# Kernel tuning notes

Measured on AMD Instinct MI355X. Metric: run time of the kernel, lower is better.

## Reference

```python
import jax, jax.numpy as jnp
import numpy as np

B, T, V, E, H = 4096, 80, 80, 8, 256  # batch, seq_len, num_classes/vocab, embed dim, n_hidden
FORGET_BIAS = 1.0  # tf BasicLSTMCell default


def lstm_layer(x, W, b):
    """Run one BasicLSTMCell layer over time. x: [B, T, D]; W: [D+H, 4H]; b: [4H].
    TF BasicLSTMCell gate order is (i, j, f, o); new_c = c*sig(f+fb) + sig(i)*tanh(j)."""
    Bsz = x.shape[0]

    def step(carry, xt):
        c, h = carry
        gates = jnp.concatenate([xt, h], axis=-1) @ W + b  # [B, 4H]
        i, j, f, o = jnp.split(gates, 4, axis=-1)
        c = c * jax.nn.sigmoid(f + FORGET_BIAS) + jax.nn.sigmoid(i) * jnp.tanh(j)
        h = jnp.tanh(c) * jax.nn.sigmoid(o)
        return (c, h), h

    init = (jnp.zeros((Bsz, H), x.dtype), jnp.zeros((Bsz, H), x.dtype))
    _, hs = jax.lax.scan(step, init, jnp.swapaxes(x, 0, 1))  # hs: [T, B, H]
    return jnp.swapaxes(hs, 0, 1)  # [B, T, H]


def setup_inputs() -> dict:
    key = jax.random.key(0)
    ks = jax.random.split(key, 8)
    features = jax.random.randint(ks[0], (B, T), 0, V, dtype=jnp.int32)
    labels = jax.random.randint(ks[1], (B,), 0, V, dtype=jnp.int32)
    emb = jax.random.normal(ks[2], (V, E), dtype=jnp.float32) * 0.1  # trainable=False in original
    W1 = jax.random.normal(ks[3], (E + H, 4 * H), dtype=jnp.float32) * 0.05
    b1 = jnp.zeros((4 * H,), jnp.float32)
    W2 = jax.random.normal(ks[4], (H + H, 4 * H), dtype=jnp.float32) * 0.05
    b2 = jnp.zeros((4 * H,), jnp.float32)
    Wd = jax.random.normal(ks[5], (H, V), dtype=jnp.float32) * 0.05
    bd = jnp.zeros((V,), jnp.float32)
    return {"features": features, "labels": labels, "emb": emb,
            "W1": W1, "b1": b1, "W2": W2, "b2": b2, "Wd": Wd, "bd": bd}


def reference(features, labels, emb, W1, b1, W2, b2, Wd, bd):
    x = emb[features]                     # [B, T, E] embedding lookup
    h1 = lstm_layer(x, W1, b1)            # [B, T, H]
    h2 = lstm_layer(h1, W2, b2)           # [B, T, H]
    pred = h2[:, -1, :] @ Wd + bd         # [B, V] logits from last timestep
    y = jax.nn.one_hot(labels, V, dtype=pred.dtype)
    loss = jnp.mean(jnp.sum(-y * jax.nn.log_softmax(pred, axis=-1), axis=-1))
    return loss
```

## Files before the change

### kernel.cpp

```cpp
#include <hip/hip_runtime.h>
#include <math.h>

#define B_SZ 4096
#define T_SZ 80
#define V_SZ 80
#define E_SZ 8
#define H_SZ 256
#define G4   1024

typedef __attribute__((ext_vector_type(8))) short short8;
typedef __attribute__((ext_vector_type(4))) float f32x4;

__device__ __forceinline__ float sigm(float x) {
    return 1.f / (1.f + __expf(-x));
}
__device__ __forceinline__ float tanhfast(float x) {
    x = fminf(fmaxf(x, -15.f), 15.f);
    float t = __expf(-2.f * x);
    return (1.f - t) / (1.f + t);
}
__device__ __forceinline__ ushort f2bf(float f) {
    unsigned u = __float_as_uint(f);
    u = (u + 0x7fffu + ((u >> 16) & 1u)) >> 16;
    return (ushort)u;
}

__global__ __launch_bounds__(256) void g1_kernel(const float* __restrict__ emb,
                                                 const float* __restrict__ W1,
                                                 const float* __restrict__ b1,
                                                 float* __restrict__ G1) {
    int idx = blockIdx.x * 256 + threadIdx.x;
    if (idx >= V_SZ * G4) return;
    int v = idx >> 10, col = idx & 1023;
    float g = b1[col];
#pragma unroll
    for (int e = 0; e < E_SZ; e++)
        g += emb[v * E_SZ + e] * W1[e * G4 + col];
    G1[idx] = g;
}

__global__ __launch_bounds__(256) void wtrans(const float* __restrict__ src, int k0,
                                              int Kshift, ushort* __restrict__ out) {
    const int K = 1 << Kshift;
    int idx = blockIdx.x * 256 + threadIdx.x;
    int n = idx >> Kshift, k = idx & (K - 1);
    out[idx] = f2bf(src[(size_t)(k0 + k) * G4 + n]);
}

__global__ __launch_bounds__(256) void wdtrans(const float* __restrict__ src,
                                               ushort* __restrict__ out) {
    int idx = blockIdx.x * 256 + threadIdx.x;
    if (idx >= V_SZ * H_SZ) return;
    int v = idx >> 8, h = idx & 255;
    out[idx] = f2bf(src[h * V_SZ + v]);
}

__global__ __launch_bounds__(256) void lstm_fused(
    const ushort* __restrict__ A1h, int Kend1,
    const int*   __restrict__ feat,
    const float* __restrict__ G1,
    float* __restrict__ c1, ushort* __restrict__ h1out,
    const ushort* __restrict__ A2x, const ushort* __restrict__ A2h, int Kend2,
    const float* __restrict__ b2,
    float* __restrict__ c2, ushort* __restrict__ h2out,
    const ushort* __restrict__ W1t, const ushort* __restrict__ W2t) {

    const int z = blockIdx.z;
    const int Kend = z ? Kend2 : Kend1;
    if (Kend < 0) return;
    const int K = z ? 512 : 256;
    const ushort* __restrict__ Wt = z ? W2t : W1t;

    __shared__ ushort As[2][128 * 40];
    __shared__ ushort Ws[2][128 * 40];

    const int tid = threadIdx.x;
    const int w = tid >> 6, l = tid & 63;
    const int l15 = l & 15, l4 = l >> 4;
    const int m0 = blockIdx.x * 128;
    const int h0 = blockIdx.y * 32;

    const int row0 = tid >> 2, c40 = tid & 3;
    const int row1 = row0 + 64;
    const int ncol0 = (row0 >> 5) * 256 + h0 + (row0 & 31);
    const int ncol1 = (row1 >> 5) * 256 + h0 + (row1 & 31);
    const size_t wbase0 = (size_t)ncol0 * K + c40 * 8;
    const size_t wbase1 = (size_t)ncol1 * K + c40 * 8;
    const int lA0 = row0 * 40 + c40 * 8, lA1 = row1 * 40 + c40 * 8;

    const int aoff0 = (w * 32 + l15) * 40 + l4 * 8;
    const int aoff1 = aoff0 + 16 * 40;
    const int boff  = l15 * 40 + l4 * 8;

    f32x4 acc[2][8];
    const f32x4 zero4 = {0.f, 0.f, 0.f, 0.f};
#pragma unroll
    for (int fg = 0; fg < 2; fg++)
#pragma unroll
        for (int cf = 0; cf < 8; cf++) acc[fg][cf] = zero4;

    auto loadTile = [&](int kt, short8& a0, short8& a1, short8& w0, short8& w1) {
        const ushort* Asrc; int kl;
        if (!z)            { Asrc = A1h; kl = kt; }
        else if (kt < 256) { Asrc = A2x; kl = kt; }
        else               { Asrc = A2h; kl = kt - 256; }
        a0 = *(const short8*)(Asrc + (size_t)(m0 + row0) * H_SZ + kl + c40 * 8);
        a1 = *(const short8*)(Asrc + (size_t)(m0 + row1) * H_SZ + kl + c40 * 8);
        w0 = *(const short8*)(Wt + wbase0 + kt);
        w1 = *(const short8*)(Wt + wbase1 + kt);
    };

    short8 ga0, ga1, gw0, gw1;
    if (Kend > 0) {
        loadTile(0, ga0, ga1, gw0, gw1);
        *(short8*)(As[0] + lA0) = ga0;
        *(short8*)(As[0] + lA1) = ga1;
        *(short8*)(Ws[0] + lA0) = gw0;
        *(short8*)(Ws[0] + lA1) = gw1;
        if (Kend > 32) loadTile(32, ga0, ga1, gw0, gw1);
        __syncthreads();
    }

    int cur = 0;
    for (int kt = 0; kt < Kend; kt += 32) {
        short8 a0 = *(const short8*)(As[cur] + aoff0);
        short8 a1 = *(const short8*)(As[cur] + aoff1);
        short8 bq[8];
#pragma unroll
        for (int cf = 0; cf < 8; cf++)
            bq[cf] = *(const short8*)(Ws[cur] + boff + cf * 640);

        __builtin_amdgcn_s_setprio(1);
#pragma unroll
        for (int cf = 0; cf < 8; cf++) {
            acc[0][cf] = __builtin_amdgcn_mfma_f32_16x16x32_bf16(a0, bq[cf], acc[0][cf], 0, 0, 0);
            acc[1][cf] = __builtin_amdgcn_mfma_f32_16x16x32_bf16(a1, bq[cf], acc[1][cf], 0, 0, 0);
        }
        __builtin_amdgcn_s_setprio(0);

        if (kt + 32 < Kend) {
            *(short8*)(As[cur ^ 1] + lA0) = ga0;
            *(short8*)(As[cur ^ 1] + lA1) = ga1;
            *(short8*)(Ws[cur ^ 1] + lA0) = gw0;
            *(short8*)(Ws[cur ^ 1] + lA1) = gw1;
            if (kt + 64 < Kend) loadTile(kt + 64, ga0, ga1, gw0, gw1);
        }
        __syncthreads();
        cur ^= 1;
    }

    float* __restrict__ cbuf = z ? c2 : c1;
    ushort* __restrict__ hout = z ? h2out : h1out;
    const bool cz = z ? (Kend == 256) : (Kend == 0);

#pragma unroll
    for (int fg = 0; fg < 2; fg++) {
#pragma unroll
        for (int r = 0; r < 4; r++) {
            const int grow = m0 + w * 32 + fg * 16 + l4 * 4 + r;
            const float* gb = z ? b2 : (G1 + (size_t)feat[(size_t)grow * T_SZ] * G4);
#pragma unroll
            for (int h16 = 0; h16 < 2; h16++) {
                const int hcol = h0 + h16 * 16 + l15;
                float gi = acc[fg][0 + h16][r] + gb[hcol];
                float gj = acc[fg][2 + h16][r] + gb[256 + hcol];
                float gf = acc[fg][4 + h16][r] + gb[512 + hcol];
                float go = acc[fg][6 + h16][r] + gb[768 + hcol];
                const size_t ci = (size_t)grow * H_SZ + hcol;
                float cp = cz ? 0.f : cbuf[ci];
                float cn = cp * sigm(gf + 1.f) + sigm(gi) * tanhfast(gj);
                float hn = tanhfast(cn) * sigm(go);
                cbuf[ci] = cn;
                hout[ci] = f2bf(hn);
            }
        }
    }
}

__global__ __launch_bounds__(256) void dense_loss(const ushort* __restrict__ h2,
                                                  const ushort* __restrict__ WdT,
                                                  const float* __restrict__ bd,
                                                  const int* __restrict__ labels,
                                                  float* __restrict__ out) {
    const int tid = threadIdx.x;
    const int w = tid >> 6, l = tid & 63;
    const int l15 = l & 15, l4 = l >> 4;
    const int m0 = blockIdx.x * 64 + w * 16;

    f32x4 acc[5];
    const f32x4 zero4 = {0.f, 0.f, 0.f, 0.f};
#pragma unroll
    for (int cf = 0; cf < 5; cf++) acc[cf] = zero4;

    for (int kt = 0; kt < 256; kt += 32) {
        short8 a = *(const short8*)(h2 + (size_t)(m0 + l15) * H_SZ + l4 * 8 + kt);
#pragma unroll
        for (int cf = 0; cf < 5; cf++) {
            short8 b = *(const short8*)(WdT + (size_t)(cf * 16 + l15) * H_SZ + l4 * 8 + kt);
            acc[cf] = __builtin_amdgcn_mfma_f32_16x16x32_bf16(a, b, acc[cf], 0, 0, 0);
        }
    }
#pragma unroll
    for (int cf = 0; cf < 5; cf++) {
        float bv = bd[cf * 16 + l15];
#pragma unroll
        for (int r = 0; r < 4; r++) acc[cf][r] += bv;
    }

#pragma unroll
    for (int r = 0; r < 4; r++) {
        const int row = m0 + l4 * 4 + r;
        float mx = acc[0][r];
#pragma unroll
        for (int cf = 1; cf < 5; cf++) mx = fmaxf(mx, acc[cf][r]);
#pragma unroll
        for (int msk = 1; msk < 16; msk <<= 1)
            mx = fmaxf(mx, __shfl_xor(mx, msk, 64));
        float s = 0.f;
#pragma unroll
        for (int cf = 0; cf < 5; cf++) s += __expf(acc[cf][r] - mx);
#pragma unroll
        for (int msk = 1; msk < 16; msk <<= 1)
            s += __shfl_xor(s, msk, 64);
        const int lab = labels[row];
        float pl = 0.f;
#pragma unroll
        for (int cf = 0; cf < 5; cf++)
            pl += (cf * 16 + l15 == lab) ? acc[cf][r] : 0.f;
#pragma unroll
        for (int msk = 1; msk < 16; msk <<= 1)
            pl += __shfl_xor(pl, msk, 64);
        if (l15 == 0)
            atomicAdd(out, (logf(s) + mx - pl) * (1.0f / B_SZ));
    }
}

extern "C" void kernel_launch(void* const* d_in, const int* in_sizes, int n_in,
                              void* d_out, int out_size, void* d_ws, size_t ws_size,
                              hipStream_t stream) {
    const int*   features = (const int*)d_in[0];
    const int*   labels   = (const int*)d_in[1];
    const float* emb      = (const float*)d_in[2];
    const float* W1       = (const float*)d_in[3];
    const float* b1       = (const float*)d_in[4];
    const float* W2       = (const float*)d_in[5];
    const float* b2       = (const float*)d_in[6];
    const float* Wd       = (const float*)d_in[7];
    const float* bd       = (const float*)d_in[8];
    float* out = (float*)d_out;

    char* base = (char*)d_ws;
    float*  G1v = (float*)base;                      base += (size_t)V_SZ * G4 * 4;
    float*  c1  = (float*)base;                      base += (size_t)B_SZ * H_SZ * 4;
    float*  c2  = (float*)base;                      base += (size_t)B_SZ * H_SZ * 4;
    ushort* h1b[2]; ushort* h2b[2];
    h1b[0] = (ushort*)base;                          base += (size_t)B_SZ * H_SZ * 2;
    h1b[1] = (ushort*)base;                          base += (size_t)B_SZ * H_SZ * 2;
    h2b[0] = (ushort*)base;                          base += (size_t)B_SZ * H_SZ * 2;
    h2b[1] = (ushort*)base;                          base += (size_t)B_SZ * H_SZ * 2;
    ushort* W1t = (ushort*)base;                     base += (size_t)G4 * H_SZ * 2;
    ushort* W2t = (ushort*)base;                     base += (size_t)G4 * 2 * H_SZ * 2;
    ushort* WdT = (ushort*)base;                     base += (size_t)V_SZ * H_SZ * 2;

    (void)hipMemsetAsync(d_out, 0, sizeof(float), stream);
    g1_kernel<<<(V_SZ * G4 + 255) / 256, 256, 0, stream>>>(emb, W1, b1, G1v);
    wtrans<<<(G4 * 256) / 256, 256, 0, stream>>>(W1, E_SZ, 8, W1t);
    wtrans<<<(G4 * 512) / 256, 256, 0, stream>>>(W2, 0, 9, W2t);
    wdtrans<<<(V_SZ * H_SZ + 255) / 256, 256, 0, stream>>>(Wd, WdT);

    dim3 grid(B_SZ / 128, H_SZ / 32, 2), blk(256);
    for (int t = 0; t <= T_SZ; t++) {
        const int Kend1 = (t < T_SZ) ? (t ? 256 : 0) : -1;
        const int Kend2 = (t >= 1) ? ((t >= 2) ? 512 : 256) : -1;
        lstm_fused<<<grid, blk, 0, stream>>>(
            (t && t < T_SZ) ? h1b[(t - 1) & 1] : nullptr, Kend1,
            features + t, G1v, c1, h1b[t & 1],
            (t >= 1) ? h1b[(t - 1) & 1] : nullptr,
            (t >= 2) ? h2b[(t - 2) & 1] : nullptr, Kend2,
            b2, c2, (t >= 1) ? h2b[(t - 1) & 1] : nullptr,
            W1t, W2t);
    }
    dense_loss<<<B_SZ / 64, 256, 0, stream>>>(h2b[(T_SZ - 1) & 1], WdT, bd, labels, out);
}
```

Measured before the change: 1.589 ms.

## Replace per-timestep launches with persistent LSTM kernel using flag-based inter-block sync

Replaces the 81 per-timestep kernel launches with a single persistent kernel of 512 blocks that loops over time. Blocks synchronise through per-(timestep, layer, batch-group) atomic counters with spin-waits and L2 writeback. Cell state moves from global memory into registers, and the LDS row stride is widened to 72. This removes launch overhead and c-state global traffic, but it relies on every block being co-resident, and the spin-wait has a timeout that could silently break correctness.

Result: slower. 3.626 ms (+128.3%).

```diff
diff --git a/kernel.cpp b/kernel.cpp
--- a/kernel.cpp
+++ b/kernel.cpp
@@ -7,6 +7,7 @@
 #define E_SZ 8
 #define H_SZ 256
 #define G4   1024
+#define S72  72
 
 typedef __attribute__((ext_vector_type(8))) short short8;
 typedef __attribute__((ext_vector_type(4))) float f32x4;
@@ -23,6 +24,23 @@
     unsigned u = __float_as_uint(f);
     u = (u + 0x7fffu + ((u >> 16) & 1u)) >> 16;
     return (ushort)u;
+}
+
+__device__ __forceinline__ short8 bp16(const ushort* p) {
+    union { unsigned long long u[2]; short8 v; } r;
+    r.u[0] = __hip_atomic_load((const unsigned long long*)p,
+                               __ATOMIC_RELAXED, __HIP_MEMORY_SCOPE_AGENT);
+    r.u[1] = __hip_atomic_load((const unsigned long long*)p + 1,
+                               __ATOMIC_RELAXED, __HIP_MEMORY_SCOPE_AGENT);
+    return r.v;
+}
+
+__device__ __forceinline__ void spin_ge(const int* f, int target) {
+    int n = 0;
+    while (__hip_atomic_load(f, __ATOMIC_RELAXED, __HIP_MEMORY_SCOPE_AGENT) < target) {
+        __builtin_amdgcn_s_sleep(2);
+        if (++n > (1 << 20)) break;
+    }
 }
 
 __global__ __launch_bounds__(256) void g1_kernel(const float* __restrict__ emb,
@@ -55,124 +73,152 @@
     out[idx] = f2bf(src[h * V_SZ + v]);
 }
 
-__global__ __launch_bounds__(256) void lstm_fused(
-    const ushort* __restrict__ A1h, int Kend1,
+__global__ __launch_bounds__(256) void lstm_persist(
     const int*   __restrict__ feat,
     const float* __restrict__ G1,
-    float* __restrict__ c1, ushort* __restrict__ h1out,
-    const ushort* __restrict__ A2x, const ushort* __restrict__ A2h, int Kend2,
     const float* __restrict__ b2,
-    float* __restrict__ c2, ushort* __restrict__ h2out,
-    const ushort* __restrict__ W1t, const ushort* __restrict__ W2t) {
-
-    const int z = blockIdx.z;
-    const int Kend = z ? Kend2 : Kend1;
-    if (Kend < 0) return;
-    const int K = z ? 512 : 256;
-    const ushort* __restrict__ Wt = z ? W2t : W1t;
-
-    __shared__ ushort As[2][128 * 40];
-    __shared__ ushort Ws[2][128 * 40];
-
+    ushort* h1a, ushort* h1bb, ushort* h2a, ushort* h2bb,
+    const ushort* __restrict__ W1t, const ushort* __restrict__ W2t,
+    int* flags) {
+
+    __shared__ __align__(16) ushort As[2][128 * S72];
+    __shared__ __align__(16) ushort Ws[2][128 * S72];
+
+    const int z  = blockIdx.z;
+    const int g  = blockIdx.y;
+    const int m0 = g * 128;
+    const int h0 = blockIdx.x * 32;
     const int tid = threadIdx.x;
     const int w = tid >> 6, l = tid & 63;
     const int l15 = l & 15, l4 = l >> 4;
-    const int m0 = blockIdx.x * 128;
-    const int h0 = blockIdx.y * 32;
+
+    const int K = z ? 512 : 256;
+    const ushort* __restrict__ Wt = z ? W2t : W1t;
 
     const int row0 = tid >> 2, c40 = tid & 3;
     const int row1 = row0 + 64;
     const int ncol0 = (row0 >> 5) * 256 + h0 + (row0 & 31);
     const int ncol1 = (row1 >> 5) * 256 + h0 + (row1 & 31);
-    const size_t wbase0 = (size_t)ncol0 * K + c40 * 8;
-    const size_t wbase1 = (size_t)ncol1 * K + c40 * 8;
-    const int lA0 = row0 * 40 + c40 * 8, lA1 = row1 * 40 + c40 * 8;
-
-    const int aoff0 = (w * 32 + l15) * 40 + l4 * 8;
-    const int aoff1 = aoff0 + 16 * 40;
-    const int boff  = l15 * 40 + l4 * 8;
-
-    f32x4 acc[2][8];
+    const size_t wb0 = (size_t)ncol0 * K + c40 * 8;
+    const size_t wb1 = (size_t)ncol1 * K + c40 * 8;
+    const int lA0 = row0 * S72 + c40 * 8, lA1 = row1 * S72 + c40 * 8;
+
+    const int aoff0 = (w * 32 + l15) * S72 + l4 * 8;
+    const int aoff1 = aoff0 + 16 * S72;
+    const int boff  = l15 * S72 + l4 * 8;
+
+    ushort* h1buf[2] = {h1a, h1bb};
+    ushort* h2buf[2] = {h2a, h2bb};
+
+    float creg[16];
+#pragma unroll
+    for (int i = 0; i < 16; i++) creg[i] = 0.f;
+
     const f32x4 zero4 = {0.f, 0.f, 0.f, 0.f};
-#pragma unroll
-    for (int fg = 0; fg < 2; fg++)
-#pragma unroll
-        for (int cf = 0; cf < 8; cf++) acc[fg][cf] = zero4;
-
-    auto loadTile = [&](int kt, short8& a0, short8& a1, short8& w0, short8& w1) {
-        const ushort* Asrc; int kl;
-        if (!z)            { Asrc = A1h; kl = kt; }
-        else if (kt < 256) { Asrc = A2x; kl = kt; }
-        else               { Asrc = A2h; kl = kt - 256; }
-        a0 = *(const short8*)(Asrc + (size_t)(m0 + row0) * H_SZ + kl + c40 * 8);
-        a1 = *(const short8*)(Asrc + (size_t)(m0 + row1) * H_SZ + kl + c40 * 8);
-        w0 = *(const short8*)(Wt + wbase0 + kt);
-        w1 = *(const short8*)(Wt + wbase1 + kt);
-    };
-
-    short8 ga0, ga1, gw0, gw1;
-    if (Kend > 0) {
-        loadTile(0, ga0, ga1, gw0, gw1);
-        *(short8*)(As[0] + lA0) = ga0;
-        *(short8*)(As[0] + lA1) = ga1;
-        *(short8*)(Ws[0] + lA0) = gw0;
-        *(short8*)(Ws[0] + lA1) = gw1;
-        if (Kend > 32) loadTile(32, ga0, ga1, gw0, gw1);
+
+    for (int t = 0; t < T_SZ; t++) {
+        if (tid == 0) {
+            if (!z) {
+                if (t >= 1) spin_ge(&flags[((t - 1) * 2 + 0) * 32 + g], 8);
+                if (t >= 2) spin_ge(&flags[((t - 2) * 2 + 1) * 32 + g], 8);
+            } else {
+                spin_ge(&flags[(t * 2 + 0) * 32 + g], 8);
+                if (t >= 1) spin_ge(&flags[((t - 1) * 2 + 1) * 32 + g], 8);
+            }
+        }
         __syncthreads();
-    }
-
-    int cur = 0;
-    for (int kt = 0; kt < Kend; kt += 32) {
-        short8 a0 = *(const short8*)(As[cur] + aoff0);
-        short8 a1 = *(const short8*)(As[cur] + aoff1);
-        short8 bq[8];
-#pragma unroll
-        for (int cf = 0; cf < 8; cf++)
-            bq[cf] = *(const short8*)(Ws[cur] + boff + cf * 640);
-
-        __builtin_amdgcn_s_setprio(1);
-#pragma unroll
-        for (int cf = 0; cf < 8; cf++) {
-            acc[0][cf] = __builtin_amdgcn_mfma_f32_16x16x32_bf16(a0, bq[cf], acc[0][cf], 0, 0, 0);
-            acc[1][cf] = __builtin_amdgcn_mfma_f32_16x16x32_bf16(a1, bq[cf], acc[1][cf], 0, 0, 0);
-        }
-        __builtin_amdgcn_s_setprio(0);
-
-        if (kt + 32 < Kend) {
-            *(short8*)(As[cur ^ 1] + lA0) = ga0;
-            *(short8*)(As[cur ^ 1] + lA1) = ga1;
-            *(short8*)(Ws[cur ^ 1] + lA0) = gw0;
-            *(short8*)(Ws[cur ^ 1] + lA1) = gw1;
-            if (kt + 64 < Kend) loadTile(kt + 64, ga0, ga1, gw0, gw1);
-        }
+
+        const int Kend = z ? (t ? 512 : 256) : (t ? 256 : 0);
+        const ushort* A1 = z ? h1buf[t & 1] : h1buf[(t + 1) & 1];
+        const ushort* A2 = h2buf[(t + 1) & 1];
+
+        f32x4 acc[2][8];
+#pragma unroll
+        for (int fg = 0; fg < 2; fg++)
+#pragma unroll
+            for (int cf = 0; cf < 8; cf++) acc[fg][cf] = zero4;
+
+        auto loadTile = [&](int kt, short8& a0, short8& a1, short8& w0, short8& w1) {
+            const ushort* Asrc; int kl;
+            if (!z || kt < 256) { Asrc = A1; kl = kt; }
+            else                { Asrc = A2; kl = kt - 256; }
+            a0 = bp16(Asrc + (size_t)(m0 + row0) * H_SZ + kl + c40 * 8);
+            a1 = bp16(Asrc + (size_t)(m0 + row1) * H_SZ + kl + c40 * 8);
+            w0 = *(const short8*)(Wt + wb0 + kt);
+            w1 = *(const short8*)(Wt + wb1 + kt);
+        };
+
+        short8 ga0, ga1, gw0, gw1;
+        if (Kend > 0) {
+            loadTile(0, ga0, ga1, gw0, gw1);
+            *(short8*)(As[0] + lA0) = ga0;
+            *(short8*)(As[0] + lA1) = ga1;
+            *(short8*)(Ws[0] + lA0) = gw0;
+            *(short8*)(Ws[0] + lA1) = gw1;
+            if (Kend > 32) loadTile(32, ga0, ga1, gw0, gw1);
+            __syncthreads();
+        }
+
+        int cur = 0;
+        for (int kt = 0; kt < Kend; kt += 32) {
+            short8 a0 = *(const short8*)(As[cur] + aoff0);
+            short8 a1 = *(const short8*)(As[cur] + aoff1);
+            short8 bq[8];
+#pragma unroll
+            for (int cf = 0; cf < 8; cf++)
+                bq[cf] = *(const short8*)(Ws[cur] + boff + cf * (16 * S72));
+
+            __builtin_amdgcn_s_setprio(1);
+#pragma unroll
+            for (int cf = 0; cf < 8; cf++) {
+                acc[0][cf] = __builtin_amdgcn_mfma_f32_16x16x32_bf16(a0, bq[cf], acc[0][cf], 0, 0, 0);
+                acc[1][cf] = __builtin_amdgcn_mfma_f32_16x16x32_bf16(a1, bq[cf], acc[1][cf], 0, 0, 0);
+            }
+            __builtin_amdgcn_s_setprio(0);
+
+            if (kt + 32 < Kend) {
+                *(short8*)(As[cur ^ 1] + lA0) = ga0;
+                *(short8*)(As[cur ^ 1] + lA1) = ga1;
+                *(short8*)(Ws[cur ^ 1] + lA0) = gw0;
+                *(short8*)(Ws[cur ^ 1] + lA1) = gw1;
+                if (kt + 64 < Kend) loadTile(kt + 64, ga0, ga1, gw0, gw1);
+            }
+            __syncthreads();
+            cur ^= 1;
+        }
+
+        ushort* hout = z ? h2buf[t & 1] : h1buf[t & 1];
+        const bool cz = (t == 0);
+
+#pragma unroll
+        for (int fg = 0; fg < 2; fg++) {
+#pragma unroll
+            for (int r = 0; r < 4; r++) {
+                const int grow = m0 + w * 32 + fg * 16 + l4 * 4 + r;
+                const float* gb = z ? b2 : (G1 + (size_t)feat[(size_t)grow * T_SZ + t] * G4);
+#pragma unroll
+                for (int h16 = 0; h16 < 2; h16++) {
+                    const int hcol = h0 + h16 * 16 + l15;
+                    float gi = acc[fg][0 + h16][r] + gb[hcol];
+                    float gj = acc[fg][2 + h16][r] + gb[256 + hcol];
+                    float gf = acc[fg][4 + h16][r] + gb[512 + hcol];
+                    float go = acc[fg][6 + h16][r] + gb[768 + hcol];
+                    const int cidx = (fg * 4 + r) * 2 + h16;
+                    float cp = cz ? 0.f : creg[cidx];
+                    float cn = cp * sigm(gf + 1.f) + sigm(gi) * tanhfast(gj);
+                    float hn = tanhfast(cn) * sigm(go);
+                    creg[cidx] = cn;
+                    hout[(size_t)grow * H_SZ + hcol] = f2bf(hn);
+                }
+            }
+        }
+
         __syncthreads();
-        cur ^= 1;
-    }
-
-    float* __restrict__ cbuf = z ? c2 : c1;
-    ushort* __restrict__ hout = z ? h2out : h1out;
-    const bool cz = z ? (Kend == 256) : (Kend == 0);
-
-#pragma unroll
-    for (int fg = 0; fg < 2; fg++) {
-#pragma unroll
-        for (int r = 0; r < 4; r++) {
-            const int grow = m0 + w * 32 + fg * 16 + l4 * 4 + r;
-            const float* gb = z ? b2 : (G1 + (size_t)feat[(size_t)grow * T_SZ] * G4);
-#pragma unroll
-            for (int h16 = 0; h16 < 2; h16++) {
-                const int hcol = h0 + h16 * 16 + l15;
-                float gi = acc[fg][0 + h16][r] + gb[hcol];
-                float gj = acc[fg][2 + h16][r] + gb[256 + hcol];
-                float gf = acc[fg][4 + h16][r] + gb[512 + hcol];
-                float go = acc[fg][6 + h16][r] + gb[768 + hcol];
-                const size_t ci = (size_t)grow * H_SZ + hcol;
-                float cp = cz ? 0.f : cbuf[ci];
-                float cn = cp * sigm(gf + 1.f) + sigm(gi) * tanhfast(gj);
-                float hn = tanhfast(cn) * sigm(go);
-                cbuf[ci] = cn;
-                hout[ci] = f2bf(hn);
-            }
+        if (tid == 0) {
+            asm volatile("buffer_wbl2 sc1" ::: "memory");
+            asm volatile("s_waitcnt vmcnt(0)" ::: "memory");
+            __hip_atomic_fetch_add(&flags[(t * 2 + z) * 32 + g], 1,
+                                   __ATOMIC_RELAXED, __HIP_MEMORY_SCOPE_AGENT);
         }
     }
 }
@@ -250,35 +296,27 @@
     float* out = (float*)d_out;
 
     char* base = (char*)d_ws;
-    float*  G1v = (float*)base;                      base += (size_t)V_SZ * G4 * 4;
-    float*  c1  = (float*)base;                      base += (size_t)B_SZ * H_SZ * 4;
-    float*  c2  = (float*)base;                      base += (size_t)B_SZ * H_SZ * 4;
-    ushort* h1b[2]; ushort* h2b[2];
-    h1b[0] = (ushort*)base;                          base += (size_t)B_SZ * H_SZ * 2;
-    h1b[1] = (ushort*)base;                          base += (size_t)B_SZ * H_SZ * 2;
-    h2b[0] = (ushort*)base;                          base += (size_t)B_SZ * H_SZ * 2;
-    h2b[1] = (ushort*)base;                          base += (size_t)B_SZ * H_SZ * 2;
-    ushort* W1t = (ushort*)base;                     base += (size_t)G4 * H_SZ * 2;
-    ushort* W2t = (ushort*)base;                     base += (size_t)G4 * 2 * H_SZ * 2;
-    ushort* WdT = (ushort*)base;                     base += (size_t)V_SZ * H_SZ * 2;
+    float*  G1v = (float*)base;      base += (size_t)V_SZ * G4 * 4;
+    ushort* h1a = (ushort*)base;     base += (size_t)B_SZ * H_SZ * 2;
+    ushort* h1b = (ushort*)base;     base += (size_t)B_SZ * H_SZ * 2;
+    ushort* h2a = (ushort*)base;     base += (size_t)B_SZ * H_SZ * 2;
+    ushort* h2b = (ushort*)base;     base += (size_t)B_SZ * H_SZ * 2;
+    ushort* W1t = (ushort*)base;     base += (size_t)G4 * H_SZ * 2;
+    ushort* W2t = (ushort*)base;     base += (size_t)G4 * 2 * H_SZ * 2;
+    ushort* WdT = (ushort*)base;     base += (size_t)V_SZ * H_SZ * 2;
+    int*    flags = (int*)base;      base += (size_t)T_SZ * 2 * 32 * 4;
 
     (void)hipMemsetAsync(d_out, 0, sizeof(float), stream);
+    (void)hipMemsetAsync(flags, 0, (size_t)T_SZ * 2 * 32 * 4, stream);
+
     g1_kernel<<<(V_SZ * G4 + 255) / 256, 256, 0, stream>>>(emb, W1, b1, G1v);
     wtrans<<<(G4 * 256) / 256, 256, 0, stream>>>(W1, E_SZ, 8, W1t);
     wtrans<<<(G4 * 512) / 256, 256, 0, stream>>>(W2, 0, 9, W2t);
     wdtrans<<<(V_SZ * H_SZ + 255) / 256, 256, 0, stream>>>(Wd, WdT);
 
-    dim3 grid(B_SZ / 128, H_SZ / 32, 2), blk(256);
-    for (int t = 0; t <= T_SZ; t++) {
-        const int Kend1 = (t < T_SZ) ? (t ? 256 : 0) : -1;
-        const int Kend2 = (t >= 1) ? ((t >= 2) ? 512 : 256) : -1;
-        lstm_fused<<<grid, blk, 0, stream>>>(
-            (t && t < T_SZ) ? h1b[(t - 1) & 1] : nullptr, Kend1,
-            features + t, G1v, c1, h1b[t & 1],
-            (t >= 1) ? h1b[(t - 1) & 1] : nullptr,
-            (t >= 2) ? h2b[(t - 2) & 1] : nullptr, Kend2,
-            b2, c2, (t >= 1) ? h2b[(t - 1) & 1] : nullptr,
-            W1t, W2t);
-    }
-    dense_loss<<<B_SZ / 64, 256, 0, stream>>>(h2b[(T_SZ - 1) & 1], WdT, bd, labels, out);
-}
+    lstm_persist<<<dim3(8, 32, 2), 256, 0, stream>>>(
+        features, G1v, b2, h1a, h1b, h2a, h2b, W1t, W2t, flags);
+
+    dense_loss<<<B_SZ / 64, 256, 0, stream>>>(h2b[0] ? (const ushort*)((T_SZ - 1) & 1 ? h2b : h2a) : h2a,
+                                              WdT, bd, labels, out);
+}
```

## Stage GEMM tiles via direct global-to-LDS loads with fragment-ordered weights

Applied to the files above, without the earlier changes.

Replaces the register-staged global loads plus LDS stores with global_load_lds DMA into shared memory. Weights are pre-packed into an MFMA-fragment-ordered layout so that each lane's 16-byte chunk lands where the MFMA read expects it, and the padded 40-stride layout is dropped. The grid axes are swapped so that blocks sharing the same batch rows are adjacent in launch order. This is meant to cut VGPR pressure and instruction overhead in the per-timestep GEMM. In exchange, the unpadded LDS layout may cause bank conflicts, and prefetch now relies on implicit waits at the barrier.

New measurement: 1.891 ms. 19.1% more time.

```diff
diff --git a/kernel.cpp b/kernel.cpp
--- a/kernel.cpp
+++ b/kernel.cpp
@@ -10,6 +10,13 @@
 
 typedef __attribute__((ext_vector_type(8))) short short8;
 typedef __attribute__((ext_vector_type(4))) float f32x4;
+
+typedef __attribute__((address_space(1))) const unsigned gu32;
+typedef __attribute__((address_space(3))) unsigned su32;
+
+__device__ __forceinline__ void glds16(const ushort* g, ushort* l) {
+    __builtin_amdgcn_global_load_lds((gu32*)g, (su32*)l, 16, 0, 0);
+}
 
 __device__ __forceinline__ float sigm(float x) {
     return 1.f / (1.f + __expf(-x));
@@ -39,12 +46,18 @@
     G1[idx] = g;
 }
 
-__global__ __launch_bounds__(256) void wtrans(const float* __restrict__ src, int k0,
-                                              int Kshift, ushort* __restrict__ out) {
-    const int K = 1 << Kshift;
+__global__ __launch_bounds__(256) void wtransf(const float* __restrict__ src, int k0,
+                                               int KTmask, int KTsh,
+                                               ushort* __restrict__ out) {
     int idx = blockIdx.x * 256 + threadIdx.x;
-    int n = idx >> Kshift, k = idx & (K - 1);
-    out[idx] = f2bf(src[(size_t)(k0 + k) * G4 + n]);
+    int j = idx & 7;
+    int c = (idx >> 3) & 511;
+    int ktile = (idx >> 12) & KTmask;
+    int hb = idx >> (12 + KTsh);
+    int cf = c >> 6;
+    int k = k0 + ktile * 32 + ((c >> 4) & 3) * 8 + j;
+    int ncol = (cf >> 1) * 256 + hb * 32 + (cf & 1) * 16 + (c & 15);
+    out[idx] = f2bf(src[(size_t)k * G4 + ncol]);
 }
 
 __global__ __launch_bounds__(256) void wdtrans(const float* __restrict__ src,
@@ -63,34 +76,33 @@
     const ushort* __restrict__ A2x, const ushort* __restrict__ A2h, int Kend2,
     const float* __restrict__ b2,
     float* __restrict__ c2, ushort* __restrict__ h2out,
-    const ushort* __restrict__ W1t, const ushort* __restrict__ W2t) {
+    const ushort* __restrict__ W1f, const ushort* __restrict__ W2f) {
 
     const int z = blockIdx.z;
     const int Kend = z ? Kend2 : Kend1;
     if (Kend < 0) return;
-    const int K = z ? 512 : 256;
-    const ushort* __restrict__ Wt = z ? W2t : W1t;
-
-    __shared__ ushort As[2][128 * 40];
-    __shared__ ushort Ws[2][128 * 40];
+    const int KT = z ? 16 : 8;
+    const ushort* __restrict__ Wf = z ? W2f : W1f;
+
+    __shared__ __align__(16) ushort As[2][4096];
+    __shared__ __align__(16) ushort Ws[2][4096];
 
     const int tid = threadIdx.x;
     const int w = tid >> 6, l = tid & 63;
     const int l15 = l & 15, l4 = l >> 4;
-    const int m0 = blockIdx.x * 128;
-    const int h0 = blockIdx.y * 32;
-
-    const int row0 = tid >> 2, c40 = tid & 3;
-    const int row1 = row0 + 64;
-    const int ncol0 = (row0 >> 5) * 256 + h0 + (row0 & 31);
-    const int ncol1 = (row1 >> 5) * 256 + h0 + (row1 & 31);
-    const size_t wbase0 = (size_t)ncol0 * K + c40 * 8;
-    const size_t wbase1 = (size_t)ncol1 * K + c40 * 8;
-    const int lA0 = row0 * 40 + c40 * 8, lA1 = row1 * 40 + c40 * 8;
-
-    const int aoff0 = (w * 32 + l15) * 40 + l4 * 8;
-    const int aoff1 = aoff0 + 16 * 40;
-    const int boff  = l15 * 40 + l4 * 8;
+    const int m0 = blockIdx.y * 128;
+    const int hb = blockIdx.x;
+    const int h0 = hb * 32;
+
+    const int rowS0 = w * 32 + l15;
+    const int rowS1 = w * 32 + 16 + l15;
+    const int kq8 = l4 * 8;
+    const int S0 = w * 2, S1 = w * 2 + 1;
+    const size_t wtileb = (size_t)hb * KT * 512;
+
+    const int aoff0 = (w * 128 + l) * 8;
+    const int aoff1 = (w * 128 + 64 + l) * 8;
+    const int boff  = l * 8;
 
     f32x4 acc[2][8];
     const f32x4 zero4 = {0.f, 0.f, 0.f, 0.f};
@@ -99,54 +111,41 @@
 #pragma unroll
         for (int cf = 0; cf < 8; cf++) acc[fg][cf] = zero4;
 
-    auto loadTile = [&](int kt, short8& a0, short8& a1, short8& w0, short8& w1) {
+    auto stage = [&](int buf, int kt) {
         const ushort* Asrc; int kl;
-        if (!z)            { Asrc = A1h; kl = kt; }
-        else if (kt < 256) { Asrc = A2x; kl = kt; }
-        else               { Asrc = A2h; kl = kt - 256; }
-        a0 = *(const short8*)(Asrc + (size_t)(m0 + row0) * H_SZ + kl + c40 * 8);
-        a1 = *(const short8*)(Asrc + (size_t)(m0 + row1) * H_SZ + kl + c40 * 8);
-        w0 = *(const short8*)(Wt + wbase0 + kt);
-        w1 = *(const short8*)(Wt + wbase1 + kt);
+        if (!z || kt < 256) { Asrc = z ? A2x : A1h; kl = kt; }
+        else                { Asrc = A2h; kl = kt - 256; }
+        glds16(Asrc + (size_t)(m0 + rowS0) * H_SZ + kl + kq8, As[buf] + S0 * 512);
+        glds16(Asrc + (size_t)(m0 + rowS1) * H_SZ + kl + kq8, As[buf] + S1 * 512);
+        const ushort* wsrc = Wf + (wtileb + (size_t)(kt >> 5) * 512) * 8;
+        glds16(wsrc + (S0 * 64 + l) * 8, Ws[buf] + S0 * 512);
+        glds16(wsrc + (S1 * 64 + l) * 8, Ws[buf] + S1 * 512);
     };
 
-    short8 ga0, ga1, gw0, gw1;
     if (Kend > 0) {
-        loadTile(0, ga0, ga1, gw0, gw1);
-        *(short8*)(As[0] + lA0) = ga0;
-        *(short8*)(As[0] + lA1) = ga1;
-        *(short8*)(Ws[0] + lA0) = gw0;
-        *(short8*)(Ws[0] + lA1) = gw1;
-        if (Kend > 32) loadTile(32, ga0, ga1, gw0, gw1);
+        stage(0, 0);
         __syncthreads();
-    }
-
-    int cur = 0;
-    for (int kt = 0; kt < Kend; kt += 32) {
-        short8 a0 = *(const short8*)(As[cur] + aoff0);
-        short8 a1 = *(const short8*)(As[cur] + aoff1);
-        short8 bq[8];
-#pragma unroll
-        for (int cf = 0; cf < 8; cf++)
-            bq[cf] = *(const short8*)(Ws[cur] + boff + cf * 640);
-
-        __builtin_amdgcn_s_setprio(1);
-#pragma unroll
-        for (int cf = 0; cf < 8; cf++) {
-            acc[0][cf] = __builtin_amdgcn_mfma_f32_16x16x32_bf16(a0, bq[cf], acc[0][cf], 0, 0, 0);
-            acc[1][cf] = __builtin_amdgcn_mfma_f32_16x16x32_bf16(a1, bq[cf], acc[1][cf], 0, 0, 0);
+        int cur = 0;
+        for (int kt = 0; kt < Kend; kt += 32) {
+            if (kt + 32 < Kend) stage(cur ^ 1, kt + 32);
+
+            short8 a0 = *(const short8*)(As[cur] + aoff0);
+            short8 a1 = *(const short8*)(As[cur] + aoff1);
+            short8 bq[8];
+#pragma unroll
+            for (int cf = 0; cf < 8; cf++)
+                bq[cf] = *(const short8*)(Ws[cur] + cf * 512 + boff);
+
+            __builtin_amdgcn_s_setprio(1);
+#pragma unroll
+            for (int cf = 0; cf < 8; cf++) {
+                acc[0][cf] = __builtin_amdgcn_mfma_f32_16x16x32_bf16(a0, bq[cf], acc[0][cf], 0, 0, 0);
+                acc[1][cf] = __builtin_amdgcn_mfma_f32_16x16x32_bf16(a1, bq[cf], acc[1][cf], 0, 0, 0);
+            }
+            __builtin_amdgcn_s_setprio(0);
+            __syncthreads();
+            cur ^= 1;
         }
-        __builtin_amdgcn_s_setprio(0);
-
-        if (kt + 32 < Kend) {
-            *(short8*)(As[cur ^ 1] + lA0) = ga0;
-            *(short8*)(As[cur ^ 1] + lA1) = ga1;
-            *(short8*)(Ws[cur ^ 1] + lA0) = gw0;
-            *(short8*)(Ws[cur ^ 1] + lA1) = gw1;
-            if (kt + 64 < Kend) loadTile(kt + 64, ga0, ga1, gw0, gw1);
-        }
-        __syncthreads();
-        cur ^= 1;
     }
 
     float* __restrict__ cbuf = z ? c2 : c1;
@@ -250,25 +249,25 @@
     float* out = (float*)d_out;
 
     char* base = (char*)d_ws;
-    float*  G1v = (float*)base;                      base += (size_t)V_SZ * G4 * 4;
-    float*  c1  = (float*)base;                      base += (size_t)B_SZ * H_SZ * 4;
-    float*  c2  = (float*)base;                      base += (size_t)B_SZ * H_SZ * 4;
+    float*  G1v = (float*)base;      base += (size_t)V_SZ * G4 * 4;
+    float*  c1  = (float*)base;      base += (size_t)B_SZ * H_SZ * 4;
+    float*  c2  = (float*)base;      base += (size_t)B_SZ * H_SZ * 4;
     ushort* h1b[2]; ushort* h2b[2];
-    h1b[0] = (ushort*)base;                          base += (size_t)B_SZ * H_SZ * 2;
-    h1b[1] = (ushort*)base;                          base += (size_t)B_SZ * H_SZ * 2;
-    h2b[0] = (ushort*)base;                          base += (size_t)B_SZ * H_SZ * 2;
-    h2b[1] = (ushort*)base;                          base += (size_t)B_SZ * H_SZ * 2;
-    ushort* W1t = (ushort*)base;                     base += (size_t)G4 * H_SZ * 2;
-    ushort* W2t = (ushort*)base;                     base += (size_t)G4 * 2 * H_SZ * 2;
-    ushort* WdT = (ushort*)base;                     base += (size_t)V_SZ * H_SZ * 2;
+    h1b[0] = (ushort*)base;          base += (size_t)B_SZ * H_SZ * 2;
+    h1b[1] = (ushort*)base;          base += (size_t)B_SZ * H_SZ * 2;
+    h2b[0] = (ushort*)base;          base += (size_t)B_SZ * H_SZ * 2;
+    h2b[1] = (ushort*)base;          base += (size_t)B_SZ * H_SZ * 2;
+    ushort* W1f = (ushort*)base;     base += (size_t)8 * 8 * 512 * 8 * 2;
+    ushort* W2f = (ushort*)base;     base += (size_t)8 * 16 * 512 * 8 * 2;
+    ushort* WdT = (ushort*)base;     base += (size_t)V_SZ * H_SZ * 2;
 
     (void)hipMemsetAsync(d_out, 0, sizeof(float), stream);
     g1_kernel<<<(V_SZ * G4 + 255) / 256, 256, 0, stream>>>(emb, W1, b1, G1v);
-    wtrans<<<(G4 * 256) / 256, 256, 0, stream>>>(W1, E_SZ, 8, W1t);
-    wtrans<<<(G4 * 512) / 256, 256, 0, stream>>>(W2, 0, 9, W2t);
+    wtransf<<<(8 * 8 * 512 * 8) / 256, 256, 0, stream>>>(W1, E_SZ, 7, 3, W1f);
+    wtransf<<<(8 * 16 * 512 * 8) / 256, 256, 0, stream>>>(W2, 0, 15, 4, W2f);
     wdtrans<<<(V_SZ * H_SZ + 255) / 256, 256, 0, stream>>>(Wd, WdT);
 
-    dim3 grid(B_SZ / 128, H_SZ / 32, 2), blk(256);
+    dim3 grid(H_SZ / 32, B_SZ / 128, 2), blk(256);
     for (int t = 0; t <= T_SZ; t++) {
         const int Kend1 = (t < T_SZ) ? (t ? 256 : 0) : -1;
         const int Kend2 = (t >= 1) ? ((t >= 2) ? 512 : 256) : -1;
@@ -278,7 +277,7 @@
             (t >= 1) ? h1b[(t - 1) & 1] : nullptr,
             (t >= 2) ? h2b[(t - 2) & 1] : nullptr, Kend2,
             b2, c2, (t >= 1) ? h2b[(t - 1) & 1] : nullptr,
-            W1t, W2t);
+            W1f, W2f);
     }
     dense_loss<<<B_SZ / 64, 256, 0, stream>>>(h2b[(T_SZ - 1) & 1], WdT, bd, labels, out);
 }
```
